# Performance work log

Measured on AMD Instinct MI355X. Metric: run time of the kernel, lower is better.

Reference implementation:

```python
import jax, jax.numpy as jnp
import numpy as np

B, C, H, W = 8, 256, 64, 64


def setup_inputs() -> dict:
    key = jax.random.key(0)
    ks = jax.random.split(key, 9)
    s = 1.0 / np.sqrt(C)  # conv2d default init scale
    return {
        "foreground": jax.random.normal(ks[0], (B, C, H, W), jnp.float32),
        "background": jax.random.normal(ks[1], (B, C, H, W), jnp.float32),
        "mask": jax.random.uniform(ks[2], (B, C, H, W), jnp.float32),
        "Wq": jax.random.normal(ks[3], (C, C), jnp.float32) * s,
        "bq": jnp.zeros((C,), jnp.float32),
        "Wk": jax.random.normal(ks[4], (C, C), jnp.float32) * s,
        "bk": jnp.zeros((C,), jnp.float32),
        "Wv": jax.random.normal(ks[5], (C, C), jnp.float32) * s,
        "bv": jnp.zeros((C,), jnp.float32),
        "gamma": jnp.ones((1,), jnp.float32),
    }


def _conv1x1(x, Wt, b):
    # 1x1 conv == per-pixel channel matmul; x: [B,C,H,W], Wt: [Cout,Cin]
    return jnp.einsum('bchw,oc->bohw', x, Wt) + b[None, :, None, None]


def reference(foreground, background, mask, Wq, bq, Wk, bk, Wv, bv, gamma):
    b, c, h, w = foreground.shape
    hw = h * w
    # mask is already at feature resolution (interpolate would be identity)
    q = _conv1x1(foreground, Wq, bq).reshape(b, c, hw)   # [B,C,HW]
    k = _conv1x1(background, Wk, bk).reshape(b, c, hw)   # [B,C,HW]
    # bmm(q, k^T): channel-channel correlation [B,C,C]
    corr = jnp.einsum('bci,bdi->bcd', q, k)
    m_r = mask.reshape(b, c, hw)                          # [B,C,HW]
    # bmm(corr, m_r): mask-modulated scores [B,C,HW]
    scores = jnp.einsum('bcd,bdi->bci', corr, m_r)
    energy = jax.nn.softmax(scores, axis=-1)
    v = _conv1x1(foreground, Wv, bv).reshape(b, c, hw)
    attended = (energy * v).reshape(b, c, h, w)
    out = foreground * mask + gamma[0] * (1.0 - mask) * attended
    return out
```

## Files before the change

kernel.cpp:

```cpp
#include <hip/hip_runtime.h>
#include <math.h>

#define B_    8
#define C_    256
#define HW_   4096
#define CHW_  ((long)C_ * HW_)

#define BKT   32
#define LDH   40
#define KS    16
#define KCH   (HW_ / KS)

typedef __attribute__((ext_vector_type(8))) short bf16x8;
typedef __attribute__((ext_vector_type(4))) float f32x4;
#define MFMA_BF16(a, b, c) __builtin_amdgcn_mfma_f32_16x16x32_bf16((a), (b), (c), 0, 0, 0)

__device__ __forceinline__ void cvt_hl4(const float4 f, uint* h, uint* l) {
    uint u0 = __float_as_uint(f.x), u1 = __float_as_uint(f.y),
         u2 = __float_as_uint(f.z), u3 = __float_as_uint(f.w);
    uint h0 = (u0 + 0x8000u) & 0xFFFF0000u, h1 = (u1 + 0x8000u) & 0xFFFF0000u,
         h2 = (u2 + 0x8000u) & 0xFFFF0000u, h3 = (u3 + 0x8000u) & 0xFFFF0000u;
    h[0] = (h0 >> 16) | h1;
    h[1] = (h2 >> 16) | h3;
    float l0 = f.x - __uint_as_float(h0), l1 = f.y - __uint_as_float(h1),
          l2 = f.z - __uint_as_float(h2), l3 = f.w - __uint_as_float(h3);
    uint a0 = __float_as_uint(l0) & 0xFFFF0000u, a1 = __float_as_uint(l1) & 0xFFFF0000u,
         a2 = __float_as_uint(l2) & 0xFFFF0000u, a3 = __float_as_uint(l3) & 0xFFFF0000u;
    l[0] = (a0 >> 16) | a1;
    l[1] = (a2 >> 16) | a3;
}
__device__ __forceinline__ void cvt_h4(const float4 f, uint* h) {
    uint u0 = __float_as_uint(f.x), u1 = __float_as_uint(f.y),
         u2 = __float_as_uint(f.z), u3 = __float_as_uint(f.w);
    uint h0 = (u0 + 0x8000u) & 0xFFFF0000u, h1 = (u1 + 0x8000u) & 0xFFFF0000u,
         h2 = (u2 + 0x8000u) & 0xFFFF0000u, h3 = (u3 + 0x8000u) & 0xFFFF0000u;
    h[0] = (h0 >> 16) | h1;
    h[1] = (h2 >> 16) | h3;
}

__global__ __launch_bounds__(256) void conv_w(
    const float* __restrict__ Wv, ushort* __restrict__ Wvh)
{
    const int i = (blockIdx.x * 256 + threadIdx.x) * 4;
    float4 v = *reinterpret_cast<const float4*>(&Wv[i]);
    uint h[2];
    cvt_h4(v, h);
    *reinterpret_cast<uint2*>(&Wvh[i]) = make_uint2(h[0], h[1]);
}

__global__ __launch_bounds__(256) void conv_transpose(
    const float* __restrict__ mask, const float* __restrict__ fg,
    ushort* __restrict__ mTh, ushort* __restrict__ mTl, ushort* __restrict__ fTh)
{
    __shared__ float tile[64][65];
    const int zi = blockIdx.z;
    const bool domask = zi < B_;
    const int b = domask ? zi : zi - B_;
    const float* src = (domask ? mask : fg) + (long)b * CHW_;
    const int e0 = blockIdx.y * 64, i0 = blockIdx.x * 64;

    const int t  = threadIdx.x;
    const int tr = t >> 4, tc = (t & 15) * 4;

    #pragma unroll
    for (int j = 0; j < 4; ++j) {
        const int e = tr + j * 16;
        float4 v = *reinterpret_cast<const float4*>(&src[(long)(e0 + e) * HW_ + i0 + tc]);
        tile[e][tc + 0] = v.x; tile[e][tc + 1] = v.y;
        tile[e][tc + 2] = v.z; tile[e][tc + 3] = v.w;
    }
    __syncthreads();

    #pragma unroll
    for (int j = 0; j < 4; ++j) {
        const int i = tr + j * 16;
        float4 v = make_float4(tile[tc + 0][i], tile[tc + 1][i], tile[tc + 2][i], tile[tc + 3][i]);
        const long o = (long)b * CHW_ + (long)(i0 + i) * C_ + e0 + tc;
        if (domask) {
            uint h[2], l[2];
            cvt_hl4(v, h, l);
            *reinterpret_cast<uint2*>(&mTh[o]) = make_uint2(h[0], h[1]);
            *reinterpret_cast<uint2*>(&mTl[o]) = make_uint2(l[0], l[1]);
        } else {
            uint h[2];
            cvt_h4(v, h);
            *reinterpret_cast<uint2*>(&fTh[o]) = make_uint2(h[0], h[1]);
        }
    }
}

__global__ __launch_bounds__(256, 3) void gemm_nt_mfma(
    const float* __restrict__ F, const float* __restrict__ G,
    float* __restrict__ part,
    float* __restrict__ fsum, float* __restrict__ gsum)
{
    __shared__ ushort Ah[128 * LDH], Al[128 * LDH], Bh[128 * LDH], Bl[128 * LDH];

    const int z  = blockIdx.z;
    const int b  = z >> 4;
    const int ks = z & (KS - 1);
    const int c0 = blockIdx.y * 128;
    const int d0 = blockIdx.x * 128;
    const float* Fb = F + (long)b * CHW_ + (long)ks * KCH;
    const float* Gb = G + (long)b * CHW_ + (long)ks * KCH;
    const bool doF = (blockIdx.x == 0);
    const bool doG = (blockIdx.y == 0);

    const int t    = threadIdx.x;
    const int srow = t >> 1;
    const int sk   = (t & 1) * 16;
    const int lane = t & 63, w = t >> 6;
    const int col  = lane & 15, quad = lane >> 4;
    const int wm   = (w >> 1) * 64, wn = (w & 1) * 64;

    f32x4 acc[4][4] = {};
    float rsF = 0.0f, rsG = 0.0f;

    for (int kt = 0; kt < KCH; kt += BKT) {
        {
            const float* s = &Fb[(long)(c0 + srow) * HW_ + kt + sk];
            float4 v0 = *reinterpret_cast<const float4*>(s);
            float4 v1 = *reinterpret_cast<const float4*>(s + 4);
            float4 v2 = *reinterpret_cast<const float4*>(s + 8);
            float4 v3 = *reinterpret_cast<const float4*>(s + 12);
            if (doF) {
                rsF += (v0.x + v0.y + v0.z + v0.w) + (v1.x + v1.y + v1.z + v1.w)
                     + (v2.x + v2.y + v2.z + v2.w) + (v3.x + v3.y + v3.z + v3.w);
            }
            uint h[4], l[4];
            cvt_hl4(v0, h + 0, l + 0);
            cvt_hl4(v1, h + 2, l + 2);
            *reinterpret_cast<uint4*>(&Ah[srow * LDH + sk]) = make_uint4(h[0], h[1], h[2], h[3]);
            *reinterpret_cast<uint4*>(&Al[srow * LDH + sk]) = make_uint4(l[0], l[1], l[2], l[3]);
            cvt_hl4(v2, h + 0, l + 0);
            cvt_hl4(v3, h + 2, l + 2);
            *reinterpret_cast<uint4*>(&Ah[srow * LDH + sk + 8]) = make_uint4(h[0], h[1], h[2], h[3]);
            *reinterpret_cast<uint4*>(&Al[srow * LDH + sk + 8]) = make_uint4(l[0], l[1], l[2], l[3]);
        }
        {
            const float* s = &Gb[(long)(d0 + srow) * HW_ + kt + sk];
            float4 v0 = *reinterpret_cast<const float4*>(s);
            float4 v1 = *reinterpret_cast<const float4*>(s + 4);
            float4 v2 = *reinterpret_cast<const float4*>(s + 8);
            float4 v3 = *reinterpret_cast<const float4*>(s + 12);
            if (doG) {
                rsG += (v0.x + v0.y + v0.z + v0.w) + (v1.x + v1.y + v1.z + v1.w)
                     + (v2.x + v2.y + v2.z + v2.w) + (v3.x + v3.y + v3.z + v3.w);
            }
            uint h[4], l[4];
            cvt_hl4(v0, h + 0, l + 0);
            cvt_hl4(v1, h + 2, l + 2);
            *reinterpret_cast<uint4*>(&Bh[srow * LDH + sk]) = make_uint4(h[0], h[1], h[2], h[3]);
            *reinterpret_cast<uint4*>(&Bl[srow * LDH + sk]) = make_uint4(l[0], l[1], l[2], l[3]);
            cvt_hl4(v2, h + 0, l + 0);
            cvt_hl4(v3, h + 2, l + 2);
            *reinterpret_cast<uint4*>(&Bh[srow * LDH + sk + 8]) = make_uint4(h[0], h[1], h[2], h[3]);
            *reinterpret_cast<uint4*>(&Bl[srow * LDH + sk + 8]) = make_uint4(l[0], l[1], l[2], l[3]);
        }
        __syncthreads();

        bf16x8 bfh[4], bfl[4];
        #pragma unroll
        for (int tj = 0; tj < 4; ++tj) {
            const int r = (wn + tj * 16 + col) * LDH + quad * 8;
            bfh[tj] = *reinterpret_cast<const bf16x8*>(&Bh[r]);
            bfl[tj] = *reinterpret_cast<const bf16x8*>(&Bl[r]);
        }
        #pragma unroll
        for (int ti = 0; ti < 4; ++ti) {
            const int r = (wm + ti * 16 + col) * LDH + quad * 8;
            bf16x8 afh = *reinterpret_cast<const bf16x8*>(&Ah[r]);
            bf16x8 afl = *reinterpret_cast<const bf16x8*>(&Al[r]);
            #pragma unroll
            for (int tj = 0; tj < 4; ++tj) {
                acc[ti][tj] = MFMA_BF16(afh, bfh[tj], acc[ti][tj]);
                acc[ti][tj] = MFMA_BF16(afh, bfl[tj], acc[ti][tj]);
                acc[ti][tj] = MFMA_BF16(afl, bfh[tj], acc[ti][tj]);
            }
        }
        __syncthreads();
    }

    rsF += __shfl_xor(rsF, 1);
    rsG += __shfl_xor(rsG, 1);
    if (doF && (t & 1) == 0) atomicAdd(&fsum[b * C_ + c0 + srow], rsF);
    if (doG && (t & 1) == 0) atomicAdd(&gsum[b * C_ + d0 + srow], rsG);

    float* P = part + (long)z * C_ * C_;
    #pragma unroll
    for (int ti = 0; ti < 4; ++ti) {
        const int m = c0 + wm + ti * 16 + quad * 4;
        #pragma unroll
        for (int tj = 0; tj < 4; ++tj) {
            const int n = d0 + wn + tj * 16 + col;
            #pragma unroll
            for (int r = 0; r < 4; ++r)
                P[(long)(m + r) * C_ + n] = acc[ti][tj][r];
        }
    }
}

__global__ __launch_bounds__(256, 3) void gemm_stats_mfma(
    const ushort* __restrict__ corrh, const ushort* __restrict__ corrl,
    const ushort* __restrict__ mTh,   const ushort* __restrict__ mTl,
    float* __restrict__ pmax, float* __restrict__ psum)
{
    __shared__ ushort Ah[128 * LDH], Al[128 * LDH], Bh[128 * LDH], Bl[128 * LDH];
    __shared__ float pm[2][128], ps[2][128];

    const int b  = blockIdx.z;
    const int m0 = blockIdx.y * 128;
    const int n0 = blockIdx.x * 128;
    const ushort* Ahb = corrh + (long)b * C_ * C_;
    const ushort* Alb = corrl + (long)b * C_ * C_;
    const ushort* Bhb = mTh + (long)b * CHW_;
    const ushort* Blb = mTl + (long)b * CHW_;

    const int t    = threadIdx.x;
    const int srow = t >> 1;
    const int sk   = (t & 1) * 16;
    const int lane = t & 63, w = t >> 6;
    const int col  = lane & 15, quad = lane >> 4;
    const int wm   = (w >> 1) * 64, wn = (w & 1) * 64;

    f32x4 acc[4][4] = {};

    for (int kt = 0; kt < C_; kt += BKT) {
        const long ga = (long)(m0 + srow) * C_ + kt + sk;
        const long gb = (long)(n0 + srow) * C_ + kt + sk;
        uint4 ah0 = *reinterpret_cast<const uint4*>(&Ahb[ga]);
        uint4 ah1 = *reinterpret_cast<const uint4*>(&Ahb[ga + 8]);
        uint4 al0 = *reinterpret_cast<const uint4*>(&Alb[ga]);
        uint4 al1 = *reinterpret_cast<const uint4*>(&Alb[ga + 8]);
        uint4 bh0 = *reinterpret_cast<const uint4*>(&Bhb[gb]);
        uint4 bh1 = *reinterpret_cast<const uint4*>(&Bhb[gb + 8]);
        uint4 bl0 = *reinterpret_cast<const uint4*>(&Blb[gb]);
        uint4 bl1 = *reinterpret_cast<const uint4*>(&Blb[gb + 8]);
        *reinterpret_cast<uint4*>(&Ah[srow * LDH + sk])     = ah0;
        *reinterpret_cast<uint4*>(&Ah[srow * LDH + sk + 8]) = ah1;
        *reinterpret_cast<uint4*>(&Al[srow * LDH + sk])     = al0;
        *reinterpret_cast<uint4*>(&Al[srow * LDH + sk + 8]) = al1;
        *reinterpret_cast<uint4*>(&Bh[srow * LDH + sk])     = bh0;
        *reinterpret_cast<uint4*>(&Bh[srow * LDH + sk + 8]) = bh1;
        *reinterpret_cast<uint4*>(&Bl[srow * LDH + sk])     = bl0;
        *reinterpret_cast<uint4*>(&Bl[srow * LDH + sk + 8]) = bl1;
        __syncthreads();

        bf16x8 bfh[4], bfl[4];
        #pragma unroll
        for (int tj = 0; tj < 4; ++tj) {
            const int r = (wn + tj * 16 + col) * LDH + quad * 8;
            bfh[tj] = *reinterpret_cast<const bf16x8*>(&Bh[r]);
            bfl[tj] = *reinterpret_cast<const bf16x8*>(&Bl[r]);
        }
        #pragma unroll
        for (int ti = 0; ti < 4; ++ti) {
            const int r = (wm + ti * 16 + col) * LDH + quad * 8;
            bf16x8 afh = *reinterpret_cast<const bf16x8*>(&Ah[r]);
            bf16x8 afl = *reinterpret_cast<const bf16x8*>(&Al[r]);
            #pragma unroll
            for (int tj = 0; tj < 4; ++tj) {
                acc[ti][tj] = MFMA_BF16(afh, bfh[tj], acc[ti][tj]);
                acc[ti][tj] = MFMA_BF16(afh, bfl[tj], acc[ti][tj]);
                acc[ti][tj] = MFMA_BF16(afl, bfh[tj], acc[ti][tj]);
            }
        }
        __syncthreads();
    }

    #pragma unroll
    for (int ti = 0; ti < 4; ++ti) {
        #pragma unroll
        for (int r = 0; r < 4; ++r) {
            float mx = fmaxf(fmaxf(acc[ti][0][r], acc[ti][1][r]),
                             fmaxf(acc[ti][2][r], acc[ti][3][r]));
            mx = fmaxf(mx, __shfl_xor(mx, 1));
            mx = fmaxf(mx, __shfl_xor(mx, 2));
            mx = fmaxf(mx, __shfl_xor(mx, 4));
            mx = fmaxf(mx, __shfl_xor(mx, 8));
            float se = __expf(acc[ti][0][r] - mx) + __expf(acc[ti][1][r] - mx)
                     + __expf(acc[ti][2][r] - mx) + __expf(acc[ti][3][r] - mx);
            se += __shfl_xor(se, 1);
            se += __shfl_xor(se, 2);
            se += __shfl_xor(se, 4);
            se += __shfl_xor(se, 8);
            if (col == 0) {
                const int rb = wm + ti * 16 + quad * 4 + r;
                pm[w & 1][rb] = mx;
                ps[w & 1][rb] = se;
            }
        }
    }
    __syncthreads();
    if (t < 128) {
        const float a0 = pm[0][t], a1 = pm[1][t];
        const float gm = fmaxf(a0, a1);
        const float gs = ps[0][t] * __expf(a0 - gm) + ps[1][t] * __expf(a1 - gm);
        const long rowg = (long)b * C_ + m0 + t;
        pmax[rowg * 32 + blockIdx.x] = gm;
        psum[rowg * 32 + blockIdx.x] = gs;
    }
}

__global__ __launch_bounds__(256, 3) void gemm_fused_final(
    const ushort* __restrict__ corrh, const ushort* __restrict__ corrl,
    const ushort* __restrict__ mTh,   const ushort* __restrict__ mTl,
    const ushort* __restrict__ Wvh,   const ushort* __restrict__ fTh,
    const float* __restrict__ pmax,   const float* __restrict__ psum,
    const float* __restrict__ bv,     const float* __restrict__ fg,
    const float* __restrict__ mask,   const float* __restrict__ gamma,
    float* __restrict__ out)
{
    __shared__ ushort Ah[128 * LDH], Al[128 * LDH];
    __shared__ ushort Bh[64 * LDH],  Bl[64 * LDH];
    __shared__ float sm[128], si[128];

    const int b  = blockIdx.z;
    const int m0 = blockIdx.y * 128;
    const int n0 = blockIdx.x * 64;
    const ushort* Ahb = corrh + (long)b * C_ * C_;
    const ushort* Alb = corrl + (long)b * C_ * C_;
    const ushort* Bhb = mTh + (long)b * CHW_;
    const ushort* Blb = mTl + (long)b * CHW_;
    const ushort* Fb  = fTh + (long)b * CHW_;

    const int t     = threadIdx.x;
    const int srow  = t >> 1;
    const int sk    = (t & 1) * 16;
    const int srowB = t >> 2;
    const int skB   = (t & 3) * 8;
    const int lane  = t & 63, w = t >> 6;
    const int col   = lane & 15, quad = lane >> 4;
    const int wm    = (w >> 1) * 64, wn = (w & 1) * 32;

    if (t < 128) {
        const long rowg = (long)b * C_ + m0 + t;
        const float* pmr = pmax + rowg * 32;
        const float* psr = psum + rowg * 32;
        float gm = -INFINITY;
        #pragma unroll
        for (int i = 0; i < 32; ++i) gm = fmaxf(gm, pmr[i]);
        float gs = 0.0f;
        #pragma unroll
        for (int i = 0; i < 32; ++i) gs += psr[i] * __expf(pmr[i] - gm);
        sm[t] = gm;
        si[t] = 1.0f / gs;
    }

    f32x4 acc_s[4][2] = {};
    for (int kt = 0; kt < C_; kt += BKT) {
        const long ga = (long)(m0 + srow) * C_ + kt + sk;
        const long gb = (long)(n0 + srowB) * C_ + kt + skB;
        uint4 ah0 = *reinterpret_cast<const uint4*>(&Ahb[ga]);
        uint4 ah1 = *reinterpret_cast<const uint4*>(&Ahb[ga + 8]);
        uint4 al0 = *reinterpret_cast<const uint4*>(&Alb[ga]);
        uint4 al1 = *reinterpret_cast<const uint4*>(&Alb[ga + 8]);
        uint4 bh0 = *reinterpret_cast<const uint4*>(&Bhb[gb]);
        uint4 bl0 = *reinterpret_cast<const uint4*>(&Blb[gb]);
        __syncthreads();
        *reinterpret_cast<uint4*>(&Ah[srow * LDH + sk])     = ah0;
        *reinterpret_cast<uint4*>(&Ah[srow * LDH + sk + 8]) = ah1;
        *reinterpret_cast<uint4*>(&Al[srow * LDH + sk])     = al0;
        *reinterpret_cast<uint4*>(&Al[srow * LDH + sk + 8]) = al1;
        *reinterpret_cast<uint4*>(&Bh[srowB * LDH + skB])   = bh0;
        *reinterpret_cast<uint4*>(&Bl[srowB * LDH + skB])   = bl0;
        __syncthreads();

        bf16x8 bfh[2], bfl[2];
        #pragma unroll
        for (int tj = 0; tj < 2; ++tj) {
            const int r = (wn + tj * 16 + col) * LDH + quad * 8;
            bfh[tj] = *reinterpret_cast<const bf16x8*>(&Bh[r]);
            bfl[tj] = *reinterpret_cast<const bf16x8*>(&Bl[r]);
        }
        #pragma unroll
        for (int ti = 0; ti < 4; ++ti) {
            const int r = (wm + ti * 16 + col) * LDH + quad * 8;
            bf16x8 afh = *reinterpret_cast<const bf16x8*>(&Ah[r]);
            bf16x8 afl = *reinterpret_cast<const bf16x8*>(&Al[r]);
            #pragma unroll
            for (int tj = 0; tj < 2; ++tj) {
                acc_s[ti][tj] = MFMA_BF16(afh, bfh[tj], acc_s[ti][tj]);
                acc_s[ti][tj] = MFMA_BF16(afh, bfl[tj], acc_s[ti][tj]);
                acc_s[ti][tj] = MFMA_BF16(afl, bfh[tj], acc_s[ti][tj]);
            }
        }
    }
    __syncthreads();

    const float g = gamma[0];
    #pragma unroll
    for (int ti = 0; ti < 4; ++ti) {
        #pragma unroll
        for (int r = 0; r < 4; ++r) {
            const int lrow = wm + ti * 16 + quad * 4 + r;
            const float mx  = sm[lrow];
            const float inv = si[lrow] * g;
            #pragma unroll
            for (int tj = 0; tj < 2; ++tj)
                acc_s[ti][tj][r] = __expf(acc_s[ti][tj][r] - mx) * inv;
        }
    }

    f32x4 acc_v[4][2] = {};
    for (int kt = 0; kt < C_; kt += BKT) {
        const long ga = (long)(m0 + srow) * C_ + kt + sk;
        const long gb = (long)(n0 + srowB) * C_ + kt + skB;
        uint4 a0 = *reinterpret_cast<const uint4*>(&Wvh[ga]);
        uint4 a1 = *reinterpret_cast<const uint4*>(&Wvh[ga + 8]);
        uint4 b0 = *reinterpret_cast<const uint4*>(&Fb[gb]);
        __syncthreads();
        *reinterpret_cast<uint4*>(&Ah[srow * LDH + sk])     = a0;
        *reinterpret_cast<uint4*>(&Ah[srow * LDH + sk + 8]) = a1;
        *reinterpret_cast<uint4*>(&Bh[srowB * LDH + skB])   = b0;
        __syncthreads();

        bf16x8 bfh[2];
        #pragma unroll
        for (int tj = 0; tj < 2; ++tj)
            bfh[tj] = *reinterpret_cast<const bf16x8*>(&Bh[(wn + tj * 16 + col) * LDH + quad * 8]);
        #pragma unroll
        for (int ti = 0; ti < 4; ++ti) {
            bf16x8 afh = *reinterpret_cast<const bf16x8*>(&Ah[(wm + ti * 16 + col) * LDH + quad * 8]);
            #pragma unroll
            for (int tj = 0; tj < 2; ++tj)
                acc_v[ti][tj] = MFMA_BF16(afh, bfh[tj], acc_v[ti][tj]);
        }
    }

    #pragma unroll
    for (int ti = 0; ti < 4; ++ti) {
        const int m = m0 + wm + ti * 16 + quad * 4;
        #pragma unroll
        for (int r = 0; r < 4; ++r) {
            const float bvm = bv[m + r];
            #pragma unroll
            for (int tj = 0; tj < 2; ++tj) {
                const int n = n0 + wn + tj * 16 + col;
                const long e = (long)b * CHW_ + (long)(m + r) * HW_ + n;
                const float f  = fg[e];
                const float mk = mask[e];
                const float vv = acc_v[ti][tj][r] + bvm;
                out[e] = f * mk + (1.0f - mk) * acc_s[ti][tj][r] * vv;
            }
        }
    }
}

__global__ __launch_bounds__(256) void reduce_part(
    const float* __restrict__ part, float* __restrict__ S1)
{
    const long idx = (long)blockIdx.x * 256 + threadIdx.x;
    const int  b   = (int)(idx >> 16);
    const long e   = idx & 65535;
    const float* p = part + ((long)b * KS) * 65536 + e;
    float s = 0.0f;
    #pragma unroll
    for (int ks = 0; ks < KS; ++ks) s += p[(long)ks * 65536];
    S1[idx] = s;
}

__global__ __launch_bounds__(256) void uvw_kernel(
    const float* __restrict__ Wq, const float* __restrict__ Wk,
    const float* __restrict__ bk,
    const float* __restrict__ fsum, const float* __restrict__ gsum,
    float* __restrict__ u, float* __restrict__ wh)
{
    const int g = blockIdx.x * 256 + threadIdx.x;
    if (g < 2048) {
        const int b = g >> 8, c = g & 255;
        const float* w = Wq + (long)c * C_;
        const float* s = fsum + b * C_;
        float acc = 0.0f;
        for (int e = 0; e < C_; ++e) acc = fmaf(w[e], s[e], acc);
        u[g] = acc;
    } else {
        const int g2 = g - 2048;
        const int b = g2 >> 8, d = g2 & 255;
        const float* w = Wk + (long)d * C_;
        const float* s = gsum + b * C_;
        float acc = 0.0f;
        for (int f = 0; f < C_; ++f) acc = fmaf(w[f], s[f], acc);
        wh[g2] = acc + (float)HW_ * bk[d];
    }
}

#define BK64 16
#define LDT64 68
__global__ __launch_bounds__(256) void gemm_nt64(
    const float* __restrict__ S1, const float* __restrict__ Wk,
    float* __restrict__ T)
{
    __shared__ float As[BK64][LDT64];
    __shared__ float Bs[BK64][LDT64];
    const int r0 = blockIdx.y * 64;
    const int d0 = blockIdx.x * 64;
    const int t   = threadIdx.x;
    const int tx  = t & 15, ty = t >> 4;
    const int tx4 = tx * 4, ty4 = ty * 4;
    const int am  = t >> 2, ak4 = (t & 3) * 4;

    float acc[4][4] = {};
    for (int k0 = 0; k0 < C_; k0 += BK64) {
        float4 av = *reinterpret_cast<const float4*>(&S1[(long)(r0 + am) * C_ + k0 + ak4]);
        float4 bw = *reinterpret_cast<const float4*>(&Wk[(long)(d0 + am) * C_ + k0 + ak4]);
        As[ak4+0][am]=av.x; As[ak4+1][am]=av.y; As[ak4+2][am]=av.z; As[ak4+3][am]=av.w;
        Bs[ak4+0][am]=bw.x; Bs[ak4+1][am]=bw.y; Bs[ak4+2][am]=bw.z; Bs[ak4+3][am]=bw.w;
        __syncthreads();
        #pragma unroll
        for (int kk = 0; kk < BK64; ++kk) {
            float4 a = *reinterpret_cast<const float4*>(&As[kk][ty4]);
            float4 x = *reinterpret_cast<const float4*>(&Bs[kk][tx4]);
            const float ar[4] = {a.x,a.y,a.z,a.w};
            const float xr[4] = {x.x,x.y,x.z,x.w};
            #pragma unroll
            for (int r = 0; r < 4; ++r)
                #pragma unroll
                for (int s = 0; s < 4; ++s)
                    acc[r][s] = fmaf(ar[r], xr[s], acc[r][s]);
        }
        __syncthreads();
    }
    #pragma unroll
    for (int r = 0; r < 4; ++r) {
        float4 o; o.x=acc[r][0]; o.y=acc[r][1]; o.z=acc[r][2]; o.w=acc[r][3];
        *reinterpret_cast<float4*>(&T[(long)(r0 + ty4 + r) * C_ + d0 + tx4]) = o;
    }
}

__global__ __launch_bounds__(256) void gemm_nn64_rank1(
    const float* __restrict__ Wq, const float* __restrict__ T,
    const float* __restrict__ u,  const float* __restrict__ bk,
    const float* __restrict__ bq, const float* __restrict__ wh,
    ushort* __restrict__ corrh, ushort* __restrict__ corrl)
{
    __shared__ float As[BK64][LDT64];
    __shared__ float Bs[BK64][LDT64];
    const int b  = blockIdx.z;
    const int m0 = blockIdx.y * 64;
    const int n0 = blockIdx.x * 64;
    const float* Tb = T + (long)b * C_ * C_;

    const int t   = threadIdx.x;
    const int tx  = t & 15, ty = t >> 4;
    const int tx4 = tx * 4, ty4 = ty * 4;
    const int am  = t >> 2, ak4 = (t & 3) * 4;
    const int xk  = ty,     xn4 = tx4;

    float acc[4][4] = {};
    for (int k0 = 0; k0 < C_; k0 += BK64) {
        float4 av = *reinterpret_cast<const float4*>(&Wq[(long)(m0 + am) * C_ + k0 + ak4]);
        float4 xv = *reinterpret_cast<const float4*>(&Tb[(long)(k0 + xk) * C_ + n0 + xn4]);
        As[ak4+0][am]=av.x; As[ak4+1][am]=av.y; As[ak4+2][am]=av.z; As[ak4+3][am]=av.w;
        *reinterpret_cast<float4*>(&Bs[xk][xn4]) = xv;
        __syncthreads();
        #pragma unroll
        for (int kk = 0; kk < BK64; ++kk) {
            float4 a = *reinterpret_cast<const float4*>(&As[kk][ty4]);
            float4 x = *reinterpret_cast<const float4*>(&Bs[kk][tx4]);
            const float ar[4] = {a.x,a.y,a.z,a.w};
            const float xr[4] = {x.x,x.y,x.z,x.w};
            #pragma unroll
            for (int r = 0; r < 4; ++r)
                #pragma unroll
                for (int s = 0; s < 4; ++s)
                    acc[r][s] = fmaf(ar[r], xr[s], acc[r][s]);
        }
        __syncthreads();
    }

    float4 bkv = *reinterpret_cast<const float4*>(&bk[n0 + tx4]);
    float4 whv = *reinterpret_cast<const float4*>(&wh[b * C_ + n0 + tx4]);
    #pragma unroll
    for (int r = 0; r < 4; ++r) {
        const int m = m0 + ty4 + r;
        const float um = u[b * C_ + m];
        const float bm = bq[m];
        float4 o;
        o.x = acc[r][0] + um*bkv.x + bm*whv.x;
        o.y = acc[r][1] + um*bkv.y + bm*whv.y;
        o.z = acc[r][2] + um*bkv.z + bm*whv.z;
        o.w = acc[r][3] + um*bkv.w + bm*whv.w;
        uint h[2], l[2];
        cvt_hl4(o, h, l);
        const long e = (long)b * C_ * C_ + (long)m * C_ + n0 + tx4;
        *reinterpret_cast<uint2*>(&corrh[e]) = make_uint2(h[0], h[1]);
        *reinterpret_cast<uint2*>(&corrl[e]) = make_uint2(l[0], l[1]);
    }
}

extern "C" void kernel_launch(void* const* d_in, const int* in_sizes, int n_in,
                              void* d_out, int out_size, void* d_ws, size_t ws_size,
                              hipStream_t stream)
{
    const float* fg    = (const float*)d_in[0];
    const float* bg    = (const float*)d_in[1];
    const float* mask  = (const float*)d_in[2];
    const float* Wq    = (const float*)d_in[3];
    const float* bq    = (const float*)d_in[4];
    const float* Wk    = (const float*)d_in[5];
    const float* bk    = (const float*)d_in[6];
    const float* Wv    = (const float*)d_in[7];
    const float* bv    = (const float*)d_in[8];
    const float* gamma = (const float*)d_in[9];
    float* out = (float*)d_out;

    char* ws = (char*)d_ws;
    float*  part   = (float*)(ws);
    ushort* mTh    = (ushort*)(ws + 33554432);
    ushort* mTl    = (ushort*)(ws + 50331648);
    ushort* fTh    = (ushort*)(ws + 67108864);
    float*  S1     = (float*)(ws + 83886080);
    float*  T      = (float*)(ws + 85983232);
    ushort* corrh  = (ushort*)(ws + 88080384);
    ushort* corrl  = (ushort*)(ws + 89128960);
    ushort* Wvh    = (ushort*)(ws + 90177536);
    float*  fsum   = (float*)(ws + 90308608);
    float*  gsum   = (float*)(ws + 90316800);
    float*  u      = (float*)(ws + 90324992);
    float*  wh     = (float*)(ws + 90333184);
    float*  pmax   = (float*)(ws + 90341376);
    float*  psum   = (float*)(ws + 90603520);

    const dim3 blk(256);

    hipMemsetAsync(fsum, 0, 16384, stream);

    conv_transpose<<<dim3(HW_ / 64, C_ / 64, 2 * B_), blk, 0, stream>>>(
        mask, fg, mTh, mTl, fTh);
    conv_w<<<dim3(64), blk, 0, stream>>>(Wv, Wvh);

    gemm_nt_mfma<<<dim3(2, 2, B_ * KS), blk, 0, stream>>>(fg, bg, part, fsum, gsum);
    reduce_part<<<dim3(B_ * C_ * C_ / 256), blk, 0, stream>>>(part, S1);

    uvw_kernel<<<dim3(16), blk, 0, stream>>>(Wq, Wk, bk, fsum, gsum, u, wh);

    gemm_nt64<<<dim3(C_ / 64, B_ * C_ / 64), blk, 0, stream>>>(S1, Wk, T);
    gemm_nn64_rank1<<<dim3(4, 4, B_), blk, 0, stream>>>(Wq, T, u, bk, bq, wh, corrh, corrl);

    gemm_stats_mfma<<<dim3(HW_ / 128, C_ / 128, B_), blk, 0, stream>>>(
        corrh, corrl, mTh, mTl, pmax, psum);

    gemm_fused_final<<<dim3(HW_ / 64, C_ / 128, B_), blk, 0, stream>>>(
        corrh, corrl, mTh, mTl, Wvh, fTh, pmax, psum, bv, fg, mask, gamma, out);
}
```

Before: 286.3 us.

## Load MFMA fragments directly from global memory, dropping LDS staging in stats/final GEMMs

The stats and fused-final GEMMs now read bf16 fragments straight from global memory (L2-cached) into registers instead of staging them through shared memory, which removes the LDS stores and barriers. The stats kernel tile shrinks to 128x64, which doubles the partial max/sum slots per row and moves the psum buffer. The final kernel merges the score and V GEMM loops into one pass. In gemm_nt, rows are remapped so each thread loads a full 16-float segment of its own row, which lets the row-sum shuffle be dropped. The trade-off is more redundant global and L2 traffic per wave in exchange for fewer barriers and better occupancy.

```diff
diff --git a/kernel.cpp b/kernel.cpp
--- a/kernel.cpp
+++ b/kernel.cpp
@@ -107,8 +107,8 @@
     const bool doG = (blockIdx.y == 0);
 
     const int t    = threadIdx.x;
-    const int srow = t >> 1;
-    const int sk   = (t & 1) * 16;
+    const int srow = t & 127;
+    const int skf  = (t >> 7) * 16;
     const int lane = t & 63, w = t >> 6;
     const int col  = lane & 15, quad = lane >> 4;
     const int wm   = (w >> 1) * 64, wn = (w & 1) * 64;
@@ -118,7 +118,7 @@
 
     for (int kt = 0; kt < KCH; kt += BKT) {
         {
-            const float* s = &Fb[(long)(c0 + srow) * HW_ + kt + sk];
+            const float* s = &Fb[(long)(c0 + srow) * HW_ + kt + skf];
             float4 v0 = *reinterpret_cast<const float4*>(s);
             float4 v1 = *reinterpret_cast<const float4*>(s + 4);
             float4 v2 = *reinterpret_cast<const float4*>(s + 8);
@@ -130,15 +130,15 @@
             uint h[4], l[4];
             cvt_hl4(v0, h + 0, l + 0);
             cvt_hl4(v1, h + 2, l + 2);
-            *reinterpret_cast<uint4*>(&Ah[srow * LDH + sk]) = make_uint4(h[0], h[1], h[2], h[3]);
-            *reinterpret_cast<uint4*>(&Al[srow * LDH + sk]) = make_uint4(l[0], l[1], l[2], l[3]);
+            *reinterpret_cast<uint4*>(&Ah[srow * LDH + skf]) = make_uint4(h[0], h[1], h[2], h[3]);
+            *reinterpret_cast<uint4*>(&Al[srow * LDH + skf]) = make_uint4(l[0], l[1], l[2], l[3]);
             cvt_hl4(v2, h + 0, l + 0);
             cvt_hl4(v3, h + 2, l + 2);
-            *reinterpret_cast<uint4*>(&Ah[srow * LDH + sk + 8]) = make_uint4(h[0], h[1], h[2], h[3]);
-            *reinterpret_cast<uint4*>(&Al[srow * LDH + sk + 8]) = make_uint4(l[0], l[1], l[2], l[3]);
+            *reinterpret_cast<uint4*>(&Ah[srow * LDH + skf + 8]) = make_uint4(h[0], h[1], h[2], h[3]);
+            *reinterpret_cast<uint4*>(&Al[srow * LDH + skf + 8]) = make_uint4(l[0], l[1], l[2], l[3]);
         }
         {
-            const float* s = &Gb[(long)(d0 + srow) * HW_ + kt + sk];
+            const float* s = &Gb[(long)(d0 + srow) * HW_ + kt + skf];
             float4 v0 = *reinterpret_cast<const float4*>(s);
             float4 v1 = *reinterpret_cast<const float4*>(s + 4);
             float4 v2 = *reinterpret_cast<const float4*>(s + 8);
@@ -150,12 +150,12 @@
             uint h[4], l[4];
             cvt_hl4(v0, h + 0, l + 0);
             cvt_hl4(v1, h + 2, l + 2);
-            *reinterpret_cast<uint4*>(&Bh[srow * LDH + sk]) = make_uint4(h[0], h[1], h[2], h[3]);
-            *reinterpret_cast<uint4*>(&Bl[srow * LDH + sk]) = make_uint4(l[0], l[1], l[2], l[3]);
+            *reinterpret_cast<uint4*>(&Bh[srow * LDH + skf]) = make_uint4(h[0], h[1], h[2], h[3]);
+            *reinterpret_cast<uint4*>(&Bl[srow * LDH + skf]) = make_uint4(l[0], l[1], l[2], l[3]);
             cvt_hl4(v2, h + 0, l + 0);
             cvt_hl4(v3, h + 2, l + 2);
-            *reinterpret_cast<uint4*>(&Bh[srow * LDH + sk + 8]) = make_uint4(h[0], h[1], h[2], h[3]);
-            *reinterpret_cast<uint4*>(&Bl[srow * LDH + sk + 8]) = make_uint4(l[0], l[1], l[2], l[3]);
+            *reinterpret_cast<uint4*>(&Bh[srow * LDH + skf + 8]) = make_uint4(h[0], h[1], h[2], h[3]);
+            *reinterpret_cast<uint4*>(&Bl[srow * LDH + skf + 8]) = make_uint4(l[0], l[1], l[2], l[3]);
         }
         __syncthreads();
 
@@ -181,10 +181,8 @@
         __syncthreads();
     }
 
-    rsF += __shfl_xor(rsF, 1);
-    rsG += __shfl_xor(rsG, 1);
-    if (doF && (t & 1) == 0) atomicAdd(&fsum[b * C_ + c0 + srow], rsF);
-    if (doG && (t & 1) == 0) atomicAdd(&gsum[b * C_ + d0 + srow], rsG);
+    if (doF) atomicAdd(&fsum[b * C_ + c0 + srow], rsF);
+    if (doG) atomicAdd(&gsum[b * C_ + d0 + srow], rsG);
 
     float* P = part + (long)z * C_ * C_;
     #pragma unroll
@@ -205,81 +203,55 @@
     const ushort* __restrict__ mTh,   const ushort* __restrict__ mTl,
     float* __restrict__ pmax, float* __restrict__ psum)
 {
-    __shared__ ushort Ah[128 * LDH], Al[128 * LDH], Bh[128 * LDH], Bl[128 * LDH];
     __shared__ float pm[2][128], ps[2][128];
 
     const int b  = blockIdx.z;
     const int m0 = blockIdx.y * 128;
-    const int n0 = blockIdx.x * 128;
+    const int n0 = blockIdx.x * 64;
     const ushort* Ahb = corrh + (long)b * C_ * C_;
     const ushort* Alb = corrl + (long)b * C_ * C_;
     const ushort* Bhb = mTh + (long)b * CHW_;
     const ushort* Blb = mTl + (long)b * CHW_;
 
     const int t    = threadIdx.x;
-    const int srow = t >> 1;
-    const int sk   = (t & 1) * 16;
     const int lane = t & 63, w = t >> 6;
     const int col  = lane & 15, quad = lane >> 4;
-    const int wm   = (w >> 1) * 64, wn = (w & 1) * 64;
-
-    f32x4 acc[4][4] = {};
+    const int wm   = (w >> 1) * 64, wn = (w & 1) * 32;
+
+    f32x4 acc[4][2] = {};
 
     for (int kt = 0; kt < C_; kt += BKT) {
-        const long ga = (long)(m0 + srow) * C_ + kt + sk;
-        const long gb = (long)(n0 + srow) * C_ + kt + sk;
-        uint4 ah0 = *reinterpret_cast<const uint4*>(&Ahb[ga]);
-        uint4 ah1 = *reinterpret_cast<const uint4*>(&Ahb[ga + 8]);
-        uint4 al0 = *reinterpret_cast<const uint4*>(&Alb[ga]);
-        uint4 al1 = *reinterpret_cast<const uint4*>(&Alb[ga + 8]);
-        uint4 bh0 = *reinterpret_cast<const uint4*>(&Bhb[gb]);
-        uint4 bh1 = *reinterpret_cast<const uint4*>(&Bhb[gb + 8]);
-        uint4 bl0 = *reinterpret_cast<const uint4*>(&Blb[gb]);
-        uint4 bl1 = *reinterpret_cast<const uint4*>(&Blb[gb + 8]);
-        *reinterpret_cast<uint4*>(&Ah[srow * LDH + sk])     = ah0;
-        *reinterpret_cast<uint4*>(&Ah[srow * LDH + sk + 8]) = ah1;
-        *reinterpret_cast<uint4*>(&Al[srow * LDH + sk])     = al0;
-        *reinterpret_cast<uint4*>(&Al[srow * LDH + sk + 8]) = al1;
-        *reinterpret_cast<uint4*>(&Bh[srow * LDH + sk])     = bh0;
-        *reinterpret_cast<uint4*>(&Bh[srow * LDH + sk + 8]) = bh1;
-        *reinterpret_cast<uint4*>(&Bl[srow * LDH + sk])     = bl0;
-        *reinterpret_cast<uint4*>(&Bl[srow * LDH + sk + 8]) = bl1;
-        __syncthreads();
-
-        bf16x8 bfh[4], bfl[4];
-        #pragma unroll
-        for (int tj = 0; tj < 4; ++tj) {
-            const int r = (wn + tj * 16 + col) * LDH + quad * 8;
-            bfh[tj] = *reinterpret_cast<const bf16x8*>(&Bh[r]);
-            bfl[tj] = *reinterpret_cast<const bf16x8*>(&Bl[r]);
+        bf16x8 bh[2], bl[2];
+        #pragma unroll
+        for (int tj = 0; tj < 2; ++tj) {
+            const long ob = (long)(n0 + wn + tj * 16 + col) * C_ + kt + quad * 8;
+            bh[tj] = *reinterpret_cast<const bf16x8*>(&Bhb[ob]);
+            bl[tj] = *reinterpret_cast<const bf16x8*>(&Blb[ob]);
         }
         #pragma unroll
         for (int ti = 0; ti < 4; ++ti) {
-            const int r = (wm + ti * 16 + col) * LDH + quad * 8;
-            bf16x8 afh = *reinterpret_cast<const bf16x8*>(&Ah[r]);
-            bf16x8 afl = *reinterpret_cast<const bf16x8*>(&Al[r]);
-            #pragma unroll
-            for (int tj = 0; tj < 4; ++tj) {
-                acc[ti][tj] = MFMA_BF16(afh, bfh[tj], acc[ti][tj]);
-                acc[ti][tj] = MFMA_BF16(afh, bfl[tj], acc[ti][tj]);
-                acc[ti][tj] = MFMA_BF16(afl, bfh[tj], acc[ti][tj]);
-            }
-        }
-        __syncthreads();
+            const long oa = (long)(m0 + wm + ti * 16 + col) * C_ + kt + quad * 8;
+            bf16x8 ah = *reinterpret_cast<const bf16x8*>(&Ahb[oa]);
+            bf16x8 al = *reinterpret_cast<const bf16x8*>(&Alb[oa]);
+            #pragma unroll
+            for (int tj = 0; tj < 2; ++tj) {
+                acc[ti][tj] = MFMA_BF16(ah, bh[tj], acc[ti][tj]);
+                acc[ti][tj] = MFMA_BF16(ah, bl[tj], acc[ti][tj]);
+                acc[ti][tj] = MFMA_BF16(al, bh[tj], acc[ti][tj]);
+            }
+        }
     }
 
     #pragma unroll
     for (int ti = 0; ti < 4; ++ti) {
         #pragma unroll
         for (int r = 0; r < 4; ++r) {
-            float mx = fmaxf(fmaxf(acc[ti][0][r], acc[ti][1][r]),
-                             fmaxf(acc[ti][2][r], acc[ti][3][r]));
+            float mx = fmaxf(acc[ti][0][r], acc[ti][1][r]);
             mx = fmaxf(mx, __shfl_xor(mx, 1));
             mx = fmaxf(mx, __shfl_xor(mx, 2));
             mx = fmaxf(mx, __shfl_xor(mx, 4));
             mx = fmaxf(mx, __shfl_xor(mx, 8));
-            float se = __expf(acc[ti][0][r] - mx) + __expf(acc[ti][1][r] - mx)
-                     + __expf(acc[ti][2][r] - mx) + __expf(acc[ti][3][r] - mx);
+            float se = __expf(acc[ti][0][r] - mx) + __expf(acc[ti][1][r] - mx);
             se += __shfl_xor(se, 1);
             se += __shfl_xor(se, 2);
             se += __shfl_xor(se, 4);
@@ -297,8 +269,8 @@
         const float gm = fmaxf(a0, a1);
         const float gs = ps[0][t] * __expf(a0 - gm) + ps[1][t] * __expf(a1 - gm);
         const long rowg = (long)b * C_ + m0 + t;
-        pmax[rowg * 32 + blockIdx.x] = gm;
-        psum[rowg * 32 + blockIdx.x] = gs;
+        pmax[rowg * 64 + blockIdx.x] = gm;
+        psum[rowg * 64 + blockIdx.x] = gs;
     }
 }
 
@@ -311,8 +283,6 @@
     const float* __restrict__ mask,   const float* __restrict__ gamma,
     float* __restrict__ out)
 {
-    __shared__ ushort Ah[128 * LDH], Al[128 * LDH];
-    __shared__ ushort Bh[64 * LDH],  Bl[64 * LDH];
     __shared__ float sm[128], si[128];
 
     const int b  = blockIdx.z;
@@ -324,69 +294,51 @@
     const ushort* Blb = mTl + (long)b * CHW_;
     const ushort* Fb  = fTh + (long)b * CHW_;
 
-    const int t     = threadIdx.x;
-    const int srow  = t >> 1;
-    const int sk    = (t & 1) * 16;
-    const int srowB = t >> 2;
-    const int skB   = (t & 3) * 8;
-    const int lane  = t & 63, w = t >> 6;
-    const int col   = lane & 15, quad = lane >> 4;
-    const int wm    = (w >> 1) * 64, wn = (w & 1) * 32;
+    const int t    = threadIdx.x;
+    const int lane = t & 63, w = t >> 6;
+    const int col  = lane & 15, quad = lane >> 4;
+    const int wm   = (w >> 1) * 64, wn = (w & 1) * 32;
 
     if (t < 128) {
         const long rowg = (long)b * C_ + m0 + t;
-        const float* pmr = pmax + rowg * 32;
-        const float* psr = psum + rowg * 32;
+        const float* pmr = pmax + rowg * 64;
+        const float* psr = psum + rowg * 64;
         float gm = -INFINITY;
-        #pragma unroll
-        for (int i = 0; i < 32; ++i) gm = fmaxf(gm, pmr[i]);
+        for (int i = 0; i < 64; ++i) gm = fmaxf(gm, pmr[i]);
         float gs = 0.0f;
-        #pragma unroll
-        for (int i = 0; i < 32; ++i) gs += psr[i] * __expf(pmr[i] - gm);
+        for (int i = 0; i < 64; ++i) gs += psr[i] * __expf(pmr[i] - gm);
         sm[t] = gm;
         si[t] = 1.0f / gs;
     }
+    __syncthreads();
 
     f32x4 acc_s[4][2] = {};
+    f32x4 acc_v[4][2] = {};
+
     for (int kt = 0; kt < C_; kt += BKT) {
-        const long ga = (long)(m0 + srow) * C_ + kt + sk;
-        const long gb = (long)(n0 + srowB) * C_ + kt + skB;
-        uint4 ah0 = *reinterpret_cast<const uint4*>(&Ahb[ga]);
-        uint4 ah1 = *reinterpret_cast<const uint4*>(&Ahb[ga + 8]);
-        uint4 al0 = *reinterpret_cast<const uint4*>(&Alb[ga]);
-        uint4 al1 = *reinterpret_cast<const uint4*>(&Alb[ga + 8]);
-        uint4 bh0 = *reinterpret_cast<const uint4*>(&Bhb[gb]);
-        uint4 bl0 = *reinterpret_cast<const uint4*>(&Blb[gb]);
-        __syncthreads();
-        *reinterpret_cast<uint4*>(&Ah[srow * LDH + sk])     = ah0;
-        *reinterpret_cast<uint4*>(&Ah[srow * LDH + sk + 8]) = ah1;
-        *reinterpret_cast<uint4*>(&Al[srow * LDH + sk])     = al0;
-        *reinterpret_cast<uint4*>(&Al[srow * LDH + sk + 8]) = al1;
-        *reinterpret_cast<uint4*>(&Bh[srowB * LDH + skB])   = bh0;
-        *reinterpret_cast<uint4*>(&Bl[srowB * LDH + skB])   = bl0;
-        __syncthreads();
-
-        bf16x8 bfh[2], bfl[2];
+        bf16x8 bh[2], bl[2], bf[2];
         #pragma unroll
         for (int tj = 0; tj < 2; ++tj) {
-            const int r = (wn + tj * 16 + col) * LDH + quad * 8;
-            bfh[tj] = *reinterpret_cast<const bf16x8*>(&Bh[r]);
-            bfl[tj] = *reinterpret_cast<const bf16x8*>(&Bl[r]);
+            const long ob = (long)(n0 + wn + tj * 16 + col) * C_ + kt + quad * 8;
+            bh[tj] = *reinterpret_cast<const bf16x8*>(&Bhb[ob]);
+            bl[tj] = *reinterpret_cast<const bf16x8*>(&Blb[ob]);
+            bf[tj] = *reinterpret_cast<const bf16x8*>(&Fb[ob]);
         }
         #pragma unroll
         for (int ti = 0; ti < 4; ++ti) {
-            const int r = (wm + ti * 16 + col) * LDH + quad * 8;
-            bf16x8 afh = *reinterpret_cast<const bf16x8*>(&Ah[r]);
-            bf16x8 afl = *reinterpret_cast<const bf16x8*>(&Al[r]);
+            const long oa = (long)(m0 + wm + ti * 16 + col) * C_ + kt + quad * 8;
+            bf16x8 ah = *reinterpret_cast<const bf16x8*>(&Ahb[oa]);
+            bf16x8 al = *reinterpret_cast<const bf16x8*>(&Alb[oa]);
+            bf16x8 aw = *reinterpret_cast<const bf16x8*>(&Wvh[oa]);
             #pragma unroll
             for (int tj = 0; tj < 2; ++tj) {
-                acc_s[ti][tj] = MFMA_BF16(afh, bfh[tj], acc_s[ti][tj]);
-                acc_s[ti][tj] = MFMA_BF16(afh, bfl[tj], acc_s[ti][tj]);
-                acc_s[ti][tj] = MFMA_BF16(afl, bfh[tj], acc_s[ti][tj]);
-            }
-        }
-    }
-    __syncthreads();
+                acc_s[ti][tj] = MFMA_BF16(ah, bh[tj], acc_s[ti][tj]);
+                acc_s[ti][tj] = MFMA_BF16(ah, bl[tj], acc_s[ti][tj]);
+                acc_s[ti][tj] = MFMA_BF16(al, bh[tj], acc_s[ti][tj]);
+                acc_v[ti][tj] = MFMA_BF16(aw, bf[tj], acc_v[ti][tj]);
+            }
+        }
+    }
 
     const float g = gamma[0];
     #pragma unroll
@@ -399,32 +351,6 @@
             #pragma unroll
             for (int tj = 0; tj < 2; ++tj)
                 acc_s[ti][tj][r] = __expf(acc_s[ti][tj][r] - mx) * inv;
-        }
-    }
-
-    f32x4 acc_v[4][2] = {};
-    for (int kt = 0; kt < C_; kt += BKT) {
-        const long ga = (long)(m0 + srow) * C_ + kt + sk;
-        const long gb = (long)(n0 + srowB) * C_ + kt + skB;
-        uint4 a0 = *reinterpret_cast<const uint4*>(&Wvh[ga]);
-        uint4 a1 = *reinterpret_cast<const uint4*>(&Wvh[ga + 8]);
-        uint4 b0 = *reinterpret_cast<const uint4*>(&Fb[gb]);
-        __syncthreads();
-        *reinterpret_cast<uint4*>(&Ah[srow * LDH + sk])     = a0;
-        *reinterpret_cast<uint4*>(&Ah[srow * LDH + sk + 8]) = a1;
-        *reinterpret_cast<uint4*>(&Bh[srowB * LDH + skB])   = b0;
-        __syncthreads();
-
-        bf16x8 bfh[2];
-        #pragma unroll
-        for (int tj = 0; tj < 2; ++tj)
-            bfh[tj] = *reinterpret_cast<const bf16x8*>(&Bh[(wn + tj * 16 + col) * LDH + quad * 8]);
-        #pragma unroll
-        for (int ti = 0; ti < 4; ++ti) {
-            bf16x8 afh = *reinterpret_cast<const bf16x8*>(&Ah[(wm + ti * 16 + col) * LDH + quad * 8]);
-            #pragma unroll
-            for (int tj = 0; tj < 2; ++tj)
-                acc_v[ti][tj] = MFMA_BF16(afh, bfh[tj], acc_v[ti][tj]);
         }
     }
 
@@ -620,7 +546,7 @@
     float*  u      = (float*)(ws + 90324992);
     float*  wh     = (float*)(ws + 90333184);
     float*  pmax   = (float*)(ws + 90341376);
-    float*  psum   = (float*)(ws + 90603520);
+    float*  psum   = (float*)(ws + 90865664);
 
     const dim3 blk(256);
 
@@ -638,7 +564,7 @@
     gemm_nt64<<<dim3(C_ / 64, B_ * C_ / 64), blk, 0, stream>>>(S1, Wk, T);
     gemm_nn64_rank1<<<dim3(4, 4, B_), blk, 0, stream>>>(Wq, T, u, bk, bq, wh, corrh, corrl);
 
-    gemm_stats_mfma<<<dim3(HW_ / 128, C_ / 128, B_), blk, 0, stream>>>(
+    gemm_stats_mfma<<<dim3(HW_ / 64, C_ / 128, B_), blk, 0, stream>>>(
         corrh, corrl, mTh, mTl, pmax, psum);
 
     gemm_fused_final<<<dim3(HW_ / 64, C_ / 128, B_), blk, 0, stream>>>(
```

Result: slower. 406.0 us (+41.8%).
